# Optimization experiments

Measured on AMD Instinct MI355X. Metric: run time of the kernel, lower is better.

The kernel has to match this reference:

```python
import jax, jax.numpy as jnp
import numpy as np

H = 64  # latent_dim // 2


def _lstm_cell(x, h, c, Wih, Whh, b):
    # PyTorch gate order: i, f, g, o
    g = x @ Wih.T + h @ Whh.T + b
    i, f, gg, o = jnp.split(g, 4, axis=-1)
    c = jax.nn.sigmoid(f) * c + jax.nn.sigmoid(i) * jnp.tanh(gg)
    h = jax.nn.sigmoid(o) * jnp.tanh(c)
    return h, c


def _run_lstm(x, Wih, Whh, b):
    # x: [B, T, D] -> outputs [B, T, H], final h, c (zero-initialized state)
    B = x.shape[0]
    h0 = jnp.zeros((B, Whh.shape[1]), x.dtype)

    def step(carry, xt):
        h, c = _lstm_cell(xt, carry[0], carry[1], Wih, Whh, b)
        return (h, c), h

    (h, c), ys = jax.lax.scan(step, (h0, h0), jnp.swapaxes(x, 0, 1))
    return jnp.swapaxes(ys, 0, 1), h, c


def setup_inputs() -> dict:
    key = jax.random.key(0)
    ks = jax.random.split(key, 16)
    B, S, T, D = 512, 1024, 512, 3
    s = 1.0 / np.sqrt(H)

    def u(k, shape):
        return jax.random.uniform(k, shape, jnp.float32, -s, s)

    return {
        "src": jax.random.normal(ks[0], (B, S, D), jnp.float32),
        "trg": jax.random.normal(ks[1], (B, T, D), jnp.float32),
        "enc1_Wih": u(ks[2], (4 * H, D)),
        "enc1_Whh": u(ks[3], (4 * H, H)),
        "enc1_b": u(ks[4], (4 * H,)),
        "enc2_Wih": u(ks[5], (4 * H, H)),
        "enc2_Whh": u(ks[6], (4 * H, H)),
        "enc2_b": u(ks[7], (4 * H,)),
        "dec1_Wih": u(ks[8], (4 * H, D)),
        "dec1_Whh": u(ks[9], (4 * H, H)),
        "dec1_b": u(ks[10], (4 * H,)),
        "dec2_Wih": u(ks[11], (4 * H, H)),
        "dec2_Whh": u(ks[12], (4 * H, H)),
        "dec2_b": u(ks[13], (4 * H,)),
        "fc_W": u(ks[14], (D, H)),
        "fc_b": u(ks[15], (D,)),
    }


def reference(src, trg, enc1_Wih, enc1_Whh, enc1_b, enc2_Wih, enc2_Whh, enc2_b,
              dec1_Wih, dec1_Whh, dec1_b, dec2_Wih, dec2_Whh, dec2_b, fc_W, fc_b):
    # Encoder: two stacked LSTMs over src; keep final state of layer 2.
    y1, _, _ = _run_lstm(src, enc1_Wih, enc1_Whh, enc1_b)
    _, h, c = _run_lstm(y1, enc2_Wih, enc2_Whh, enc2_b)

    # Decoder (teacher_forcing_ratio = 1.0, the only well-defined branch):
    # at each step both decoder LSTMs share/chain the SAME (h, c) state,
    # exactly as the original Decoder.forward does with seq-len-1 inputs.
    def step(carry, xt):
        h, c = carry
        h1, c1 = _lstm_cell(xt, h, c, dec1_Wih, dec1_Whh, dec1_b)
        h2, c2 = _lstm_cell(h1, h1, c1, dec2_Wih, dec2_Whh, dec2_b)
        return (h2, c2), h2 @ fc_W.T + fc_b

    xs = jnp.swapaxes(trg[:, :-1, :], 0, 1)  # inputs for t = 1..T-1
    _, preds = jax.lax.scan(step, (h, c), xs)
    preds = jnp.swapaxes(preds, 0, 1)  # [B, T-1, 3]

    B = trg.shape[0]
    zero0 = jnp.zeros((B, 1, fc_b.shape[0]), preds.dtype)  # outputs[:, 0] stays 0
    return jnp.concatenate([zero0, preds], axis=1)
```

## Files before the change

### kernel.cpp

```cpp
#include <hip/hip_runtime.h>
#include <math.h>

typedef _Float16 f16;
typedef _Float16 f16x8 __attribute__((ext_vector_type(8)));
typedef float    f32x4 __attribute__((ext_vector_type(4)));

#define MFMA16(A, B, C) __builtin_amdgcn_mfma_f32_16x16x32_f16((A), (B), (C), 0, 0, 0)
#define LOG2E 1.44269504088896f

__device__ __forceinline__ float sig2(float a) {
    return __builtin_amdgcn_rcpf(1.0f + __builtin_amdgcn_exp2f(a));
}
__device__ __forceinline__ float tanh2(float c) {
    return fmaf(2.0f, sig2(c * (-2.0f * LOG2E)), -1.0f);
}

__device__ __forceinline__ f16x8 ldfrag(const float* __restrict__ W, int n, int k0, float s) {
    const float* p = W + (size_t)n * 64 + k0;
    f16x8 r;
#pragma unroll
    for (int j = 0; j < 8; j++) r[j] = (f16)(s * p[j]);
    return r;
}

__global__ __launch_bounds__(512, 1)
void seq2seq_kernel(const float* __restrict__ src, const float* __restrict__ trg,
                    const float* __restrict__ e1ih, const float* __restrict__ e1hh,
                    const float* __restrict__ e1b,
                    const float* __restrict__ e2ih, const float* __restrict__ e2hh,
                    const float* __restrict__ e2b,
                    const float* __restrict__ d1ih, const float* __restrict__ d1hh,
                    const float* __restrict__ d1b,
                    const float* __restrict__ d2ih, const float* __restrict__ d2hh,
                    const float* __restrict__ d2b,
                    const float* __restrict__ fcW, const float* __restrict__ fcb,
                    float* __restrict__ out)
{
    const int bp   = blockIdx.x;
    const int tid  = threadIdx.x;
    const int wv   = tid >> 6;
    const bool isB = (wv >= 4);
    const int wvg  = wv & 3;
    const int lane = tid & 63;
    const int quad = lane >> 4;
    const int c15  = lane & 15;
    const int u16  = wvg * 16 + c15;
    const int qb   = quad & 1;
    const int ab   = c15 & 1;

    __shared__ __align__(16) float xst[1024][8];
    __shared__ __align__(16) float tst[512][8];
    __shared__ __align__(16) f16 h1l[2][2][64];
    __shared__ __align__(16) f16 h2l[2][2][64];
    __shared__ float c1buf[2][64];
    __shared__ float c2buf[2][64];
    __shared__ __align__(16) f16 ring[2][16][72];
    __shared__ __align__(16) float prj[2][2][64][4];

    {
        const float* s0 = src + (size_t)(2 * bp) * 3072;
        const float* s1 = s0 + 3072;
        for (int i = tid; i < 3072; i += 512) {
            int t = i / 3, c = i - 3 * t;
            xst[t][c]     = s0[i];
            xst[t][4 + c] = s1[i];
        }
        const float* t0p = trg + (size_t)(2 * bp) * 1536;
        const float* t1p = t0p + 1536;
        for (int i = tid; i < 1536; i += 512) {
            int t = i / 3, c = i - 3 * t;
            tst[t][c]     = t0p[i];
            tst[t][4 + c] = t1p[i];
        }
    }

    f16x8 E1hh[4][2], E2ih[4][2];
    f16x8 E2hh[4][2];
    float xw[4][3], bias1[4];
    f32x4 bs2[4];
    if (!isB) {
#pragma unroll
        for (int g = 0; g < 4; g++) {
            const float s = (g == 2) ? (-2.0f * LOG2E) : (-LOG2E);
            const int n = g * 64 + u16;
#pragma unroll
            for (int c = 0; c < 2; c++) {
                E1hh[g][c] = ldfrag(e1hh, n, c * 32 + quad * 8, s);
                E2ih[g][c] = ldfrag(e2ih, n, c * 32 + quad * 8, s);
            }
            xw[g][0] = s * e1ih[n * 3 + 0];
            xw[g][1] = s * e1ih[n * 3 + 1];
            xw[g][2] = s * e1ih[n * 3 + 2];
            bias1[g] = s * e1b[n];
        }
    } else {
#pragma unroll
        for (int g = 0; g < 4; g++) {
            const float s = (g == 2) ? (-2.0f * LOG2E) : (-LOG2E);
            const int n = g * 64 + u16;
#pragma unroll
            for (int c = 0; c < 2; c++)
                E2hh[g][c] = ldfrag(e2hh, n, c * 32 + quad * 8, s);
            float bv = s * e2b[n];
            bs2[g] = (f32x4){bv, bv, bv, bv};
        }
    }

    float c1 = 0.f, c2 = 0.f;
    if (tid < 256) {
        (&h1l[0][0][0])[tid] = (f16)0.f;
        (&h2l[0][0][0])[tid] = (f16)0.f;
    }
    __syncthreads();

    const f32x4 z4 = {0.f, 0.f, 0.f, 0.f};

    f32x4 xq = z4, xnq = z4;
    if (!isB) xq = *(const f32x4*)&xst[0][qb * 4];

#pragma unroll 1
    for (int tau = 0; tau <= 1025; tau++) {
        if (!isB) {
            if (tau <= 1024) {
                const f16* h1p = h1l[(tau + 1) & 1][ab];
                f16x8 a0 = *(const f16x8*)(h1p + quad * 8);
                f16x8 a1 = *(const f16x8*)(h1p + 32 + quad * 8);
                if (tau < 1024) {
                    float xt[4];
#pragma unroll
                    for (int g = 0; g < 4; g++)
                        xt[g] = fmaf(xw[g][0], xq.x,
                                fmaf(xw[g][1], xq.y, fmaf(xw[g][2], xq.z, bias1[g])));
                    f32x4 acc[4];
#pragma unroll
                    for (int g = 0; g < 4; g++)
                        acc[g] = MFMA16(a1, E1hh[g][1], MFMA16(a0, E1hh[g][0], z4));
                    float v[4];
#pragma unroll
                    for (int g = 0; g < 4; g++)
                        v[g] = (qb ? acc[g][1] : acc[g][0]) + xt[g];
                    float iv = sig2(v[0]), fv = sig2(v[1]);
                    float gv = fmaf(2.0f, sig2(v[2]), -1.0f), ov = sig2(v[3]);
                    c1 = fv * c1 + iv * gv;
                    if (quad < 2) h1l[tau & 1][quad][u16] = (f16)(ov * tanh2(c1));
                    const int tn = (tau + 1 < 1024) ? tau + 1 : 1023;
                    xnq = *(const f32x4*)&xst[tn][qb * 4];
                }
                if (tau >= 1) {
                    f32x4 ap[4];
#pragma unroll
                    for (int g = 0; g < 4; g++)
                        ap[g] = MFMA16(a1, E2ih[g][1], MFMA16(a0, E2ih[g][0], z4));
                    if (quad < 2) {
                        f32x4 pv;
#pragma unroll
                        for (int g = 0; g < 4; g++)
                            pv[g] = qb ? ap[g][1] : ap[g][0];
                        *(f32x4*)&prj[(tau + 1) & 1][qb][u16][0] = pv;
                    }
                }
            }
        } else {
            if (tau >= 2) {
                const f16* h2p = h2l[(tau + 1) & 1][ab];
                f32x4 pj = *(const f32x4*)&prj[tau & 1][qb][u16][0];
                f16x8 b0 = *(const f16x8*)(h2p + quad * 8);
                f16x8 b1 = *(const f16x8*)(h2p + 32 + quad * 8);
                f32x4 accB[4];
#pragma unroll
                for (int g = 0; g < 4; g++)
                    accB[g] = MFMA16(b1, E2hh[g][1], MFMA16(b0, E2hh[g][0], bs2[g]));
                float v[4];
#pragma unroll
                for (int g = 0; g < 4; g++)
                    v[g] = pj[g] + (qb ? accB[g][1] : accB[g][0]);
                float iv = sig2(v[0]), fv = sig2(v[1]);
                float gv = fmaf(2.0f, sig2(v[2]), -1.0f), ov = sig2(v[3]);
                c2 = fv * c2 + iv * gv;
                if (quad < 2) h2l[tau & 1][quad][u16] = (f16)(ov * tanh2(c2));
            }
        }
        __syncthreads();
        if (!isB) xq = xnq;
    }

    f16x8 D1hh[4][2];
    f16x8 W2s[4][2];
    float dxw[4][3], db1[4];
    f32x4 db2s[4];
    if (!isB) {
#pragma unroll
        for (int g = 0; g < 4; g++) {
            const float s = (g == 2) ? (-2.0f * LOG2E) : (-LOG2E);
            const int n = g * 64 + u16;
#pragma unroll
            for (int c = 0; c < 2; c++)
                D1hh[g][c] = ldfrag(d1hh, n, c * 32 + quad * 8, s);
            dxw[g][0] = s * d1ih[n * 3 + 0];
            dxw[g][1] = s * d1ih[n * 3 + 1];
            dxw[g][2] = s * d1ih[n * 3 + 2];
            db1[g] = s * d1b[n];
        }
    } else {
#pragma unroll
        for (int g = 0; g < 4; g++) {
            const float s = (g == 2) ? (-2.0f * LOG2E) : (-LOG2E);
            const int n = g * 64 + u16;
#pragma unroll
            for (int c = 0; c < 2; c++) {
                const int k0 = c * 32 + quad * 8;
                const float* pa = d2ih + (size_t)n * 64 + k0;
                const float* pb = d2hh + (size_t)n * 64 + k0;
                f16x8 r2;
#pragma unroll
                for (int j = 0; j < 8; j++) r2[j] = (f16)(s * (pa[j] + pb[j]));
                W2s[g][c] = r2;
            }
            float bv = s * d2b[n];
            db2s[g] = (f32x4){bv, bv, bv, bv};
        }
        if (quad < 2) c2buf[quad][u16] = c2;
    }
    f16x8 FW0 = {}, FW1 = {};
    float fb = 0.f;
    if (wv >= 6 && c15 < 3) {
#pragma unroll
        for (int j = 0; j < 8; j++) {
            FW0[j] = (f16)fcW[c15 * 64 + quad * 8 + j];
            FW1[j] = (f16)fcW[c15 * 64 + 32 + quad * 8 + j];
        }
        fb = fcb[c15];
    }
    __syncthreads();

    f32x4 tq = z4, tnq = z4;
    if (!isB) tq = *(const f32x4*)&tst[0][qb * 4];

#pragma unroll 1
    for (int t = 0; t < 511; t++) {
        const int r = t & 1, w = r ^ 1;
        if (!isB) {
            const f16* hp = h2l[w][ab];
            f16x8 a0 = *(const f16x8*)(hp + quad * 8);
            f16x8 a1 = *(const f16x8*)(hp + 32 + quad * 8);
            float cdin = c2buf[qb][u16];
            float xt[4];
#pragma unroll
            for (int g = 0; g < 4; g++)
                xt[g] = fmaf(dxw[g][0], tq.x,
                        fmaf(dxw[g][1], tq.y, fmaf(dxw[g][2], tq.z, db1[g])));
            f32x4 acc[4];
#pragma unroll
            for (int g = 0; g < 4; g++)
                acc[g] = MFMA16(a1, D1hh[g][1], MFMA16(a0, D1hh[g][0], z4));
            float v[4];
#pragma unroll
            for (int g = 0; g < 4; g++)
                v[g] = (qb ? acc[g][1] : acc[g][0]) + xt[g];
            float iv = sig2(v[0]), fv = sig2(v[1]);
            float gv = fmaf(2.0f, sig2(v[2]), -1.0f), ov = sig2(v[3]);
            float c1d = fv * cdin + iv * gv;
            if (quad < 2) {
                h1l[w][quad][u16] = (f16)(ov * tanh2(c1d));
                c1buf[quad][u16]  = c1d;
            }
            const int tn = (t + 1 < 511) ? t + 1 : 510;
            tnq = *(const f32x4*)&tst[tn][qb * 4];
        } else if (wv >= 6 && t > 0 && (t & 15) == 0) {
            const int bsel = wv - 6;
            const f16* rp = &ring[bsel][0][0];
            f16x8 fa0 = *(const f16x8*)(rp + c15 * 72 + quad * 8);
            f16x8 fa1 = *(const f16x8*)(rp + c15 * 72 + 32 + quad * 8);
            f32x4 acc = MFMA16(fa1, FW1, MFMA16(fa0, FW0, z4));
            if (c15 < 3) {
                float* ob = out + (((size_t)(2 * bp + bsel) * 512 + (t - 15)) * 3) + c15;
#pragma unroll
                for (int rg = 0; rg < 4; rg++)
                    ob[(quad * 4 + rg) * 3] = acc[rg] + fb;
            }
        }
        __syncthreads();
        if (!isB) tq = tnq;

        if (isB) {
            const f16* np = h1l[w][ab];
            f16x8 m0 = *(const f16x8*)(np + quad * 8);
            f16x8 m1 = *(const f16x8*)(np + 32 + quad * 8);
            float c1in = c1buf[qb][u16];
            f32x4 acc[4];
#pragma unroll
            for (int g = 0; g < 4; g++)
                acc[g] = MFMA16(m1, W2s[g][1], MFMA16(m0, W2s[g][0], db2s[g]));
            float v[4];
#pragma unroll
            for (int g = 0; g < 4; g++)
                v[g] = (qb ? acc[g][1] : acc[g][0]);
            float i2 = sig2(v[0]), f2 = sig2(v[1]);
            float g2 = fmaf(2.0f, sig2(v[2]), -1.0f), o2 = sig2(v[3]);
            float c2d = f2 * c1in + i2 * g2;
            if (quad < 2) {
                f16 hh = (f16)(o2 * tanh2(c2d));
                h2l[r][quad][u16] = hh;
                c2buf[quad][u16]  = c2d;
                ring[quad][t & 15][u16] = hh;
            }
        }
        __syncthreads();
    }

    if (wv >= 6) {
        const int bsel = wv - 6;
        const f16* rp = &ring[bsel][0][0];
        f16x8 fa0 = *(const f16x8*)(rp + c15 * 72 + quad * 8);
        f16x8 fa1 = *(const f16x8*)(rp + c15 * 72 + 32 + quad * 8);
        f32x4 acc = MFMA16(fa1, FW1, MFMA16(fa0, FW0, z4));
        if (c15 < 3) {
            float* ob = out + (((size_t)(2 * bp + bsel) * 512 + 497) * 3) + c15;
#pragma unroll
            for (int rg = 0; rg < 4; rg++) {
                int step = quad * 4 + rg;
                if (step < 15) ob[step * 3] = acc[rg] + fb;
            }
        }
    }
}

extern "C" void kernel_launch(void* const* d_in, const int* in_sizes, int n_in,
                              void* d_out, int out_size, void* d_ws, size_t ws_size,
                              hipStream_t stream)
{
    const float* src   = (const float*)d_in[0];
    const float* trg   = (const float*)d_in[1];
    const float* e1ih  = (const float*)d_in[2];
    const float* e1hh  = (const float*)d_in[3];
    const float* e1b   = (const float*)d_in[4];
    const float* e2ih  = (const float*)d_in[5];
    const float* e2hh  = (const float*)d_in[6];
    const float* e2b   = (const float*)d_in[7];
    const float* dd1ih = (const float*)d_in[8];
    const float* dd1hh = (const float*)d_in[9];
    const float* dd1b  = (const float*)d_in[10];
    const float* dd2ih = (const float*)d_in[11];
    const float* dd2hh = (const float*)d_in[12];
    const float* dd2b  = (const float*)d_in[13];
    const float* fcW   = (const float*)d_in[14];
    const float* fcb   = (const float*)d_in[15];
    float* out = (float*)d_out;

    hipMemsetAsync(d_out, 0, (size_t)out_size * sizeof(float), stream);

    seq2seq_kernel<<<256, 512, 0, stream>>>(src, trg,
                                            e1ih, e1hh, e1b, e2ih, e2hh, e2b,
                                            dd1ih, dd1hh, dd1b, dd2ih, dd2hh, dd2b,
                                            fcW, fcb, out);
}
```

Before: 829.1 us.

## Batch encoder layer-2 input projection over 8-step windows on B-waves

Moves the enc2 input projection (h1 @ Wih2) off the critical-path A waves onto the B waves. B waves compute it in batched 8-step windows from a 16-deep h1 history ring, which lengthens the pipeline lag to 16 steps. Removes the LDS staging of src/trg and loads x directly from global memory with prefetch. Replaces __syncthreads with a raw waitcnt+s_barrier and pads the h buffers to 72 halves. This shortens the per-step serial A work at the cost of more LDS, extra B-wave work and 14 extra loop iterations.

```diff
diff --git a/kernel.cpp b/kernel.cpp
--- a/kernel.cpp
+++ b/kernel.cpp
@@ -7,6 +7,8 @@
 
 #define MFMA16(A, B, C) __builtin_amdgcn_mfma_f32_16x16x32_f16((A), (B), (C), 0, 0, 0)
 #define LOG2E 1.44269504088896f
+
+#define BAR() asm volatile("s_waitcnt lgkmcnt(0)\n\ts_barrier" ::: "memory")
 
 __device__ __forceinline__ float sig2(float a) {
     return __builtin_amdgcn_rcpf(1.0f + __builtin_amdgcn_exp2f(a));
@@ -48,34 +50,15 @@
     const int qb   = quad & 1;
     const int ab   = c15 & 1;
 
-    __shared__ __align__(16) float xst[1024][8];
-    __shared__ __align__(16) float tst[512][8];
-    __shared__ __align__(16) f16 h1l[2][2][64];
-    __shared__ __align__(16) f16 h2l[2][2][64];
+    __shared__ __align__(16) f16 h1l[16][2][72];
+    __shared__ __align__(16) f16 h2l[2][2][72];
     __shared__ float c1buf[2][64];
     __shared__ float c2buf[2][64];
     __shared__ __align__(16) f16 ring[2][16][72];
-    __shared__ __align__(16) float prj[2][2][64][4];
-
-    {
-        const float* s0 = src + (size_t)(2 * bp) * 3072;
-        const float* s1 = s0 + 3072;
-        for (int i = tid; i < 3072; i += 512) {
-            int t = i / 3, c = i - 3 * t;
-            xst[t][c]     = s0[i];
-            xst[t][4 + c] = s1[i];
-        }
-        const float* t0p = trg + (size_t)(2 * bp) * 1536;
-        const float* t1p = t0p + 1536;
-        for (int i = tid; i < 1536; i += 512) {
-            int t = i / 3, c = i - 3 * t;
-            tst[t][c]     = t0p[i];
-            tst[t][4 + c] = t1p[i];
-        }
-    }
-
-    f16x8 E1hh[4][2], E2ih[4][2];
-    f16x8 E2hh[4][2];
+    __shared__ __align__(16) float prj[16][2][64][4];
+
+    f16x8 E1hh[4][2];
+    f16x8 Wi0[4], Wi1[4], Wh0[4], Wh1[4];
     float xw[4][3], bias1[4];
     f32x4 bs2[4];
     if (!isB) {
@@ -83,11 +66,8 @@
         for (int g = 0; g < 4; g++) {
             const float s = (g == 2) ? (-2.0f * LOG2E) : (-LOG2E);
             const int n = g * 64 + u16;
-#pragma unroll
-            for (int c = 0; c < 2; c++) {
-                E1hh[g][c] = ldfrag(e1hh, n, c * 32 + quad * 8, s);
-                E2ih[g][c] = ldfrag(e2ih, n, c * 32 + quad * 8, s);
-            }
+            E1hh[g][0] = ldfrag(e1hh, n, quad * 8, s);
+            E1hh[g][1] = ldfrag(e1hh, n, 32 + quad * 8, s);
             xw[g][0] = s * e1ih[n * 3 + 0];
             xw[g][1] = s * e1ih[n * 3 + 1];
             xw[g][2] = s * e1ih[n * 3 + 2];
@@ -98,78 +78,68 @@
         for (int g = 0; g < 4; g++) {
             const float s = (g == 2) ? (-2.0f * LOG2E) : (-LOG2E);
             const int n = g * 64 + u16;
-#pragma unroll
-            for (int c = 0; c < 2; c++)
-                E2hh[g][c] = ldfrag(e2hh, n, c * 32 + quad * 8, s);
+            Wi0[g] = ldfrag(e2ih, n, quad * 8, s);
+            Wi1[g] = ldfrag(e2ih, n, 32 + quad * 8, s);
+            Wh0[g] = ldfrag(e2hh, n, quad * 8, s);
+            Wh1[g] = ldfrag(e2hh, n, 32 + quad * 8, s);
             float bv = s * e2b[n];
             bs2[g] = (f32x4){bv, bv, bv, bv};
         }
     }
 
+    { f16* z = &h1l[0][0][0]; for (int i = tid; i < 2304; i += 512) z[i] = (f16)0.f; }
+    { f16* z = &h2l[0][0][0]; for (int i = tid; i < 288;  i += 512) z[i] = (f16)0.f; }
+    __syncthreads();
+
+    const f32x4 z4 = {0.f, 0.f, 0.f, 0.f};
     float c1 = 0.f, c2 = 0.f;
-    if (tid < 256) {
-        (&h1l[0][0][0])[tid] = (f16)0.f;
-        (&h2l[0][0][0])[tid] = (f16)0.f;
-    }
-    __syncthreads();
-
-    const f32x4 z4 = {0.f, 0.f, 0.f, 0.f};
-
-    f32x4 xq = z4, xnq = z4;
-    if (!isB) xq = *(const f32x4*)&xst[0][qb * 4];
+
+    const float* xsrc = src + (size_t)(2 * bp + qb) * 3072;
+    float x0 = 0.f, x1 = 0.f, x2 = 0.f, xn0 = 0.f, xn1 = 0.f, xn2 = 0.f;
+    if (!isB) { x0 = xsrc[0]; x1 = xsrc[1]; x2 = xsrc[2]; }
+
+    f16x8 pa0 = {}, pa1 = {};
+    f32x4 pacc = z4;
 
 #pragma unroll 1
-    for (int tau = 0; tau <= 1025; tau++) {
+    for (int tau = 0; tau < 1040; tau++) {
         if (!isB) {
-            if (tau <= 1024) {
-                const f16* h1p = h1l[(tau + 1) & 1][ab];
+            if (tau < 1024) {
+                const f16* h1p = &h1l[(tau + 15) & 15][0][0] + ab * 72;
                 f16x8 a0 = *(const f16x8*)(h1p + quad * 8);
                 f16x8 a1 = *(const f16x8*)(h1p + 32 + quad * 8);
-                if (tau < 1024) {
-                    float xt[4];
-#pragma unroll
-                    for (int g = 0; g < 4; g++)
-                        xt[g] = fmaf(xw[g][0], xq.x,
-                                fmaf(xw[g][1], xq.y, fmaf(xw[g][2], xq.z, bias1[g])));
-                    f32x4 acc[4];
-#pragma unroll
-                    for (int g = 0; g < 4; g++)
-                        acc[g] = MFMA16(a1, E1hh[g][1], MFMA16(a0, E1hh[g][0], z4));
-                    float v[4];
-#pragma unroll
-                    for (int g = 0; g < 4; g++)
-                        v[g] = (qb ? acc[g][1] : acc[g][0]) + xt[g];
-                    float iv = sig2(v[0]), fv = sig2(v[1]);
-                    float gv = fmaf(2.0f, sig2(v[2]), -1.0f), ov = sig2(v[3]);
-                    c1 = fv * c1 + iv * gv;
-                    if (quad < 2) h1l[tau & 1][quad][u16] = (f16)(ov * tanh2(c1));
-                    const int tn = (tau + 1 < 1024) ? tau + 1 : 1023;
-                    xnq = *(const f32x4*)&xst[tn][qb * 4];
-                }
-                if (tau >= 1) {
-                    f32x4 ap[4];
-#pragma unroll
-                    for (int g = 0; g < 4; g++)
-                        ap[g] = MFMA16(a1, E2ih[g][1], MFMA16(a0, E2ih[g][0], z4));
-                    if (quad < 2) {
-                        f32x4 pv;
-#pragma unroll
-                        for (int g = 0; g < 4; g++)
-                            pv[g] = qb ? ap[g][1] : ap[g][0];
-                        *(f32x4*)&prj[(tau + 1) & 1][qb][u16][0] = pv;
-                    }
-                }
+                float xt[4];
+#pragma unroll
+                for (int g = 0; g < 4; g++)
+                    xt[g] = fmaf(xw[g][0], x0,
+                            fmaf(xw[g][1], x1, fmaf(xw[g][2], x2, bias1[g])));
+                f32x4 acc[4];
+#pragma unroll
+                for (int g = 0; g < 4; g++)
+                    acc[g] = MFMA16(a1, E1hh[g][1], MFMA16(a0, E1hh[g][0], z4));
+                float v[4];
+#pragma unroll
+                for (int g = 0; g < 4; g++)
+                    v[g] = (qb ? acc[g][1] : acc[g][0]) + xt[g];
+                float iv = sig2(v[0]), fv = sig2(v[1]);
+                float gv = fmaf(2.0f, sig2(v[2]), -1.0f), ov = sig2(v[3]);
+                c1 = fv * c1 + iv * gv;
+                if (quad < 2)
+                    (&h1l[tau & 15][0][0])[quad * 72 + u16] = (f16)(ov * tanh2(c1));
+                const int tn = (tau + 1 < 1024) ? tau + 1 : 1023;
+                xn0 = xsrc[tn * 3]; xn1 = xsrc[tn * 3 + 1]; xn2 = xsrc[tn * 3 + 2];
             }
         } else {
-            if (tau >= 2) {
-                const f16* h2p = h2l[(tau + 1) & 1][ab];
-                f32x4 pj = *(const f32x4*)&prj[tau & 1][qb][u16][0];
+            if (tau >= 16) {
+                const int tk = tau - 16;
+                const f16* h2p = &h2l[(tk - 1) & 1][0][0] + ab * 72;
                 f16x8 b0 = *(const f16x8*)(h2p + quad * 8);
                 f16x8 b1 = *(const f16x8*)(h2p + 32 + quad * 8);
+                f32x4 pj = *(const f32x4*)&prj[tk & 15][qb][u16][0];
                 f32x4 accB[4];
 #pragma unroll
                 for (int g = 0; g < 4; g++)
-                    accB[g] = MFMA16(b1, E2hh[g][1], MFMA16(b0, E2hh[g][0], bs2[g]));
+                    accB[g] = MFMA16(b1, Wh1[g], MFMA16(b0, Wh0[g], bs2[g]));
                 float v[4];
 #pragma unroll
                 for (int g = 0; g < 4; g++)
@@ -177,11 +147,33 @@
                 float iv = sig2(v[0]), fv = sig2(v[1]);
                 float gv = fmaf(2.0f, sig2(v[2]), -1.0f), ov = sig2(v[3]);
                 c2 = fv * c2 + iv * gv;
-                if (quad < 2) h2l[tau & 1][quad][u16] = (f16)(ov * tanh2(c2));
-            }
-        }
-        __syncthreads();
-        if (!isB) xq = xnq;
+                if (quad < 2)
+                    (&h2l[tk & 1][0][0])[quad * 72 + u16] = (f16)(ov * tanh2(c2));
+            }
+            if (tau >= 8 && tau < 1032) {
+                const int s = (tau - 8) & 7, w = (tau - 8) >> 3;
+                if (s == 0) {
+                    const int off = ((w * 8 + (c15 & 7)) & 15) * 144
+                                  + (c15 >> 3) * 72 + quad * 8;
+                    const f16* pp = &h1l[0][0][0];
+                    pa0 = *(const f16x8*)(pp + off);
+                    pa1 = *(const f16x8*)(pp + off + 32);
+                }
+                const int g = s >> 1;
+                if ((s & 1) == 0) {
+                    pacc = MFMA16(pa0, Wi0[g], z4);
+                } else {
+                    pacc = MFMA16(pa1, Wi1[g], pacc);
+#pragma unroll
+                    for (int rr = 0; rr < 4; rr++) {
+                        const int row = quad * 4 + rr;
+                        prj[(w * 8 + (row & 7)) & 15][row >> 3][u16][g] = pacc[rr];
+                    }
+                }
+            }
+        }
+        BAR();
+        if (!isB) { x0 = xn0; x1 = xn1; x2 = xn2; }
     }
 
     f16x8 D1hh[4][2];
@@ -193,9 +185,8 @@
         for (int g = 0; g < 4; g++) {
             const float s = (g == 2) ? (-2.0f * LOG2E) : (-LOG2E);
             const int n = g * 64 + u16;
-#pragma unroll
-            for (int c = 0; c < 2; c++)
-                D1hh[g][c] = ldfrag(d1hh, n, c * 32 + quad * 8, s);
+            D1hh[g][0] = ldfrag(d1hh, n, quad * 8, s);
+            D1hh[g][1] = ldfrag(d1hh, n, 32 + quad * 8, s);
             dxw[g][0] = s * d1ih[n * 3 + 0];
             dxw[g][1] = s * d1ih[n * 3 + 1];
             dxw[g][2] = s * d1ih[n * 3 + 2];
@@ -233,22 +224,23 @@
     }
     __syncthreads();
 
-    f32x4 tq = z4, tnq = z4;
-    if (!isB) tq = *(const f32x4*)&tst[0][qb * 4];
+    const float* ttrg = trg + (size_t)(2 * bp + qb) * 1536;
+    float t0v = 0.f, t1v = 0.f, t2v = 0.f, tn0 = 0.f, tn1 = 0.f, tn2 = 0.f;
+    if (!isB) { t0v = ttrg[0]; t1v = ttrg[1]; t2v = ttrg[2]; }
 
 #pragma unroll 1
     for (int t = 0; t < 511; t++) {
         const int r = t & 1, w = r ^ 1;
         if (!isB) {
-            const f16* hp = h2l[w][ab];
+            const f16* hp = &h2l[w][0][0] + ab * 72;
             f16x8 a0 = *(const f16x8*)(hp + quad * 8);
             f16x8 a1 = *(const f16x8*)(hp + 32 + quad * 8);
             float cdin = c2buf[qb][u16];
             float xt[4];
 #pragma unroll
             for (int g = 0; g < 4; g++)
-                xt[g] = fmaf(dxw[g][0], tq.x,
-                        fmaf(dxw[g][1], tq.y, fmaf(dxw[g][2], tq.z, db1[g])));
+                xt[g] = fmaf(dxw[g][0], t0v,
+                        fmaf(dxw[g][1], t1v, fmaf(dxw[g][2], t2v, db1[g])));
             f32x4 acc[4];
 #pragma unroll
             for (int g = 0; g < 4; g++)
@@ -261,11 +253,11 @@
             float gv = fmaf(2.0f, sig2(v[2]), -1.0f), ov = sig2(v[3]);
             float c1d = fv * cdin + iv * gv;
             if (quad < 2) {
-                h1l[w][quad][u16] = (f16)(ov * tanh2(c1d));
-                c1buf[quad][u16]  = c1d;
+                (&h1l[w][0][0])[quad * 72 + u16] = (f16)(ov * tanh2(c1d));
+                c1buf[quad][u16] = c1d;
             }
             const int tn = (t + 1 < 511) ? t + 1 : 510;
-            tnq = *(const f32x4*)&tst[tn][qb * 4];
+            tn0 = ttrg[tn * 3]; tn1 = ttrg[tn * 3 + 1]; tn2 = ttrg[tn * 3 + 2];
         } else if (wv >= 6 && t > 0 && (t & 15) == 0) {
             const int bsel = wv - 6;
             const f16* rp = &ring[bsel][0][0];
@@ -279,11 +271,11 @@
                     ob[(quad * 4 + rg) * 3] = acc[rg] + fb;
             }
         }
-        __syncthreads();
-        if (!isB) tq = tnq;
+        BAR();
+        if (!isB) { t0v = tn0; t1v = tn1; t2v = tn2; }
 
         if (isB) {
-            const f16* np = h1l[w][ab];
+            const f16* np = &h1l[w][0][0] + ab * 72;
             f16x8 m0 = *(const f16x8*)(np + quad * 8);
             f16x8 m1 = *(const f16x8*)(np + 32 + quad * 8);
             float c1in = c1buf[qb][u16];
@@ -300,12 +292,12 @@
             float c2d = f2 * c1in + i2 * g2;
             if (quad < 2) {
                 f16 hh = (f16)(o2 * tanh2(c2d));
-                h2l[r][quad][u16] = hh;
-                c2buf[quad][u16]  = c2d;
+                (&h2l[r][0][0])[quad * 72 + u16] = hh;
+                c2buf[quad][u16] = c2d;
                 ring[quad][t & 15][u16] = hh;
             }
         }
-        __syncthreads();
+        BAR();
     }
 
     if (wv >= 6) {
```

New measurement: 2.623 ms. 3.16x slower.
